# Optimization experiments

Hardware: AMD Instinct MI355X
Metric: run time of the kernel (lower is better)

Reference implementation:

```python
import jax, jax.numpy as jnp
import numpy as np

RATIOS = (0.5, 1.0, 2.0)
SCALES = (8.0, 16.0, 32.0)
FEAT_STRIDE = 16
BASE_SIZE = 16.0
NMS_THRESH = 0.7
N_PRE = 6000   # pre-NMS top-k (eval-mode ProposalCreator default)
N_POST = 300   # post-NMS proposals per image (eval-mode default)
MIN_SIZE = 16.0
SCALE = 1.0


def generate_anchor_base():
    ab = np.zeros((len(RATIOS) * len(SCALES), 4), np.float32)
    for i, r in enumerate(RATIOS):
        for j, s in enumerate(SCALES):
            h = BASE_SIZE * s * np.sqrt(r)
            w = BASE_SIZE * s * np.sqrt(1.0 / r)
            ab[i * len(SCALES) + j] = [-h / 2.0, -w / 2.0, h / 2.0, w / 2.0]
    return jnp.asarray(ab)


def enumerate_shifted_anchor(anchor_base, feat_stride, H, W):
    sy = jnp.arange(H, dtype=jnp.float32) * feat_stride
    sx = jnp.arange(W, dtype=jnp.float32) * feat_stride
    sx, sy = jnp.meshgrid(sx, sy)  # row-major over (y, x), matching torch permute order
    shift = jnp.stack([sy.ravel(), sx.ravel(), sy.ravel(), sx.ravel()], axis=1)  # [K,4]
    anchors = anchor_base[None, :, :] + shift[:, None, :]  # [K, A, 4]
    return anchors.reshape(-1, 4)


def loc2bbox(anchor, loc):
    # boxes in (y1, x1, y2, x2) format
    h = anchor[:, 2] - anchor[:, 0]
    w = anchor[:, 3] - anchor[:, 1]
    cy = anchor[:, 0] + 0.5 * h
    cx = anchor[:, 1] + 0.5 * w
    dy, dx, dh, dw = loc[:, 0], loc[:, 1], loc[:, 2], loc[:, 3]
    cy = cy + dy * h
    cx = cx + dx * w
    h = h * jnp.exp(dh)
    w = w * jnp.exp(dw)
    return jnp.stack([cy - 0.5 * h, cx - 0.5 * w, cy + 0.5 * h, cx + 0.5 * w], axis=1)


def nms_fixed(boxes, scores):
    # boxes [N_PRE,4] sorted desc by scores; greedy NMS emitting N_POST picks (padded)
    area = (boxes[:, 2] - boxes[:, 0]) * (boxes[:, 3] - boxes[:, 1])

    def step(sc, _):
        i = jnp.argmax(sc)
        v = sc[i] > -jnp.inf
        b = boxes[i]
        yy1 = jnp.maximum(boxes[:, 0], b[0])
        xx1 = jnp.maximum(boxes[:, 1], b[1])
        yy2 = jnp.minimum(boxes[:, 2], b[2])
        xx2 = jnp.minimum(boxes[:, 3], b[3])
        inter = jnp.maximum(yy2 - yy1, 0.0) * jnp.maximum(xx2 - xx1, 0.0)
        iou = inter / (area + area[i] - inter + 1e-9)
        sc = jnp.where((iou > NMS_THRESH) & v, -jnp.inf, sc)
        sc = sc.at[i].set(-jnp.inf)
        return sc, (i, v)

    _, (idx, valid) = jax.lax.scan(step, scores, None, length=N_POST)
    return jnp.where(valid[:, None], boxes[idx], 0.0)  # [N_POST, 4]


def proposal_one(loc, score, anchor, img_h, img_w):
    roi = loc2bbox(anchor, loc)
    roi = jnp.stack([
        jnp.clip(roi[:, 0], 0.0, img_h), jnp.clip(roi[:, 1], 0.0, img_w),
        jnp.clip(roi[:, 2], 0.0, img_h), jnp.clip(roi[:, 3], 0.0, img_w)], axis=1)
    hs = roi[:, 2] - roi[:, 0]
    ws = roi[:, 3] - roi[:, 1]
    min_size = MIN_SIZE * SCALE
    valid = (hs >= min_size) & (ws >= min_size)
    s = jnp.where(valid, score, -jnp.inf)
    top_s, top_i = jax.lax.top_k(s, N_PRE)
    return nms_fixed(roi[top_i], top_s)


def setup_inputs() -> dict:
    key = jax.random.key(0)
    ks = jax.random.split(key, 4)
    B, C, H, W = 8, 512, 64, 64
    A = 9
    return {
        "x": jax.random.normal(ks[0], (B, C, H, W), jnp.float32),
        "conv_w": jax.random.normal(ks[1], (C, C, 3, 3), jnp.float32) * 0.01,
        "conv_b": jnp.zeros((C,), jnp.float32),
        "loc_w": jax.random.normal(ks[2], (A * 4, C, 1, 1), jnp.float32) * 0.01,
        "loc_b": jnp.zeros((A * 4,), jnp.float32),
        "cls_w": jax.random.normal(ks[3], (A * 2, C, 1, 1), jnp.float32) * 0.01,
        "cls_b": jnp.zeros((A * 2,), jnp.float32),
        "img_h": 1024,
        "img_w": 1024,
    }


def reference(x, conv_w, conv_b, loc_w, loc_b, cls_w, cls_b, img_h, img_w):
    dn = ("NCHW", "OIHW", "NCHW")
    h = jax.lax.conv_general_dilated(x, conv_w, (1, 1), "SAME", dimension_numbers=dn)
    h = jax.nn.relu(h + conv_b[None, :, None, None])
    cls = jax.nn.sigmoid(
        jax.lax.conv_general_dilated(h, cls_w, (1, 1), "VALID", dimension_numbers=dn)
        + cls_b[None, :, None, None])
    loc = (jax.lax.conv_general_dilated(h, loc_w, (1, 1), "VALID", dimension_numbers=dn)
           + loc_b[None, :, None, None])
    B, _, H, W = h.shape
    anchor = enumerate_shifted_anchor(generate_anchor_base(), FEAT_STRIDE, H, W)
    pred_locations = loc.transpose(0, 2, 3, 1).reshape(B, -1, 4)          # [B, HWA, 4]
    cls_hw = cls.transpose(0, 2, 3, 1)                                     # [B, H, W, 2A]
    objectness = cls_hw.reshape(B, H, W, -1, 2)[..., 1].reshape(B, -1)     # [B, HWA]
    pred_cls_scores = cls_hw.reshape(B, -1, 2)                             # [B, HWA, 2]
    fh = jnp.float32(img_h)
    fw = jnp.float32(img_w)
    rois = jax.vmap(lambda l, s: proposal_one(l, s, anchor, fh, fw))(pred_locations, objectness)
    rois = rois.reshape(B * N_POST, 4)
    roi_indices = jnp.repeat(jnp.arange(B, dtype=jnp.int64 if jax.config.jax_enable_x64 else jnp.int32), N_POST)
    return pred_cls_scores, pred_locations, rois, roi_indices
```

## Files before the change

### kernel.cpp

```cpp
#include <hip/hip_runtime.h>
#include <cstdint>
#include <cmath>


#define AS1U(p) ((const __attribute__((address_space(1))) unsigned int*)(p))
#define AS3U(p) ((__attribute__((address_space(3))) unsigned int*)(p))

__global__ __launch_bounds__(256) void k_conv3x3(
        const float* __restrict__ x, const float* __restrict__ w,
        const float* __restrict__ bias, const float* __restrict__ zeropad,
        float* __restrict__ hout) {
    __shared__ __align__(16) float xs[8][6][68];
    __shared__ __align__(16) float wl[8][9][68];

    const int ytile = blockIdx.x;
    const int co0 = blockIdx.y * 64;
    const int b = blockIdx.z;
    const int t = threadIdx.x;
    const int xq = t & 7;
    const int coq = (t >> 3) & 7;
    const int yy = t >> 6;
    const int lane = t & 63;
    const int y0 = ytile * 4;

    if (t < 48) { int ci = t / 6, ry = t % 6; xs[ci][ry][0] = 0.f; xs[ci][ry][65] = 0.f; }

    float acc[8][8];
#pragma unroll
    for (int c = 0; c < 8; ++c)
#pragma unroll
        for (int i = 0; i < 8; ++i) acc[c][i] = 0.f;

    const int co_s = t >> 2, qs = t & 3;
    const float* wsrc = w + (size_t)(co0 + co_s) * 4608 + qs * 18;
    float* wrow = &wl[0][0][0] + (size_t)(2 * qs) * 9 * 68 + co_s;

    const int gy0 = y0 - 1;
    const float* xb = x + ((size_t)b * 512) * 4096;

    for (int ci0 = 0; ci0 < 512; ci0 += 8) {
        __syncthreads();
        {
#pragma unroll
            for (int j = 0; j < 12; ++j) {
                const int ci = 2 * yy + (j >= 6 ? 1 : 0);
                const int ry = (j >= 6) ? (j - 6) : j;
                const int gy = gy0 + ry;
                const float* src = (gy >= 0 && gy < 64)
                    ? xb + ((size_t)(ci0 + ci) * 64 + gy) * 64 + lane
                    : zeropad + lane;
                __builtin_amdgcn_global_load_lds(AS1U(src), AS3U(&xs[ci][ry][1]), 4, 0, 0);
            }
        }
        {
            const float2* wp2 = (const float2*)(wsrc + (size_t)ci0 * 9);
#pragma unroll
            for (int j2 = 0; j2 < 9; ++j2) {
                float2 f = wp2[j2];
                const int i0 = 2 * j2, i1 = 2 * j2 + 1;
                wrow[(i0 < 9 ? 0 : 9 * 68) + (i0 < 9 ? i0 : i0 - 9) * 68] = f.x;
                wrow[(i1 < 9 ? 0 : 9 * 68) + (i1 < 9 ? i1 : i1 - 9) * 68] = f.y;
            }
        }
        __syncthreads();
#pragma unroll
        for (int ci = 0; ci < 8; ++ci) {
#pragma unroll
            for (int ky = 0; ky < 3; ++ky) {
                const float* xr = &xs[ci][yy + ky][xq * 8];
                const float4 a0 = *(const float4*)(xr);
                const float4 a1 = *(const float4*)(xr + 4);
                const float2 a2 = *(const float2*)(xr + 8);
                float xw[10];
                xw[0] = a0.x; xw[1] = a0.y; xw[2] = a0.z; xw[3] = a0.w;
                xw[4] = a1.x; xw[5] = a1.y; xw[6] = a1.z; xw[7] = a1.w;
                xw[8] = a2.x; xw[9] = a2.y;
#pragma unroll
                for (int kx = 0; kx < 3; ++kx) {
                    const float4 w0 = *(const float4*)&wl[ci][ky * 3 + kx][coq * 8];
                    const float4 w1 = *(const float4*)&wl[ci][ky * 3 + kx][coq * 8 + 4];
#pragma unroll
                    for (int i = 0; i < 8; ++i) {
                        const float xv = xw[i + kx];
                        acc[0][i] += w0.x * xv; acc[1][i] += w0.y * xv;
                        acc[2][i] += w0.z * xv; acc[3][i] += w0.w * xv;
                        acc[4][i] += w1.x * xv; acc[5][i] += w1.y * xv;
                        acc[6][i] += w1.z * xv; acc[7][i] += w1.w * xv;
                    }
                }
            }
        }
    }
    const int y = y0 + yy;
#pragma unroll
    for (int c = 0; c < 8; ++c) {
        const int co = co0 + coq * 8 + c;
        const float bv = bias[co];
        float* op = hout + (((size_t)b * 512 + co) * 64 + y) * 64 + xq * 8;
        float4 o0, o1;
        o0.x = fmaxf(acc[c][0] + bv, 0.f); o0.y = fmaxf(acc[c][1] + bv, 0.f);
        o0.z = fmaxf(acc[c][2] + bv, 0.f); o0.w = fmaxf(acc[c][3] + bv, 0.f);
        o1.x = fmaxf(acc[c][4] + bv, 0.f); o1.y = fmaxf(acc[c][5] + bv, 0.f);
        o1.z = fmaxf(acc[c][6] + bv, 0.f); o1.w = fmaxf(acc[c][7] + bv, 0.f);
        *(float4*)(op) = o0;
        *(float4*)(op + 4) = o1;
    }
}

__global__ __launch_bounds__(128) void k_head(
        const float* __restrict__ h,
        const float* __restrict__ cls_w, const float* __restrict__ cls_b,
        const float* __restrict__ loc_w, const float* __restrict__ loc_b,
        const int* __restrict__ img_h_p, const int* __restrict__ img_w_p,
        float* __restrict__ out_cls, float* __restrict__ out_loc,
        float* __restrict__ boxes, float* __restrict__ scores) {
    const int tg = blockIdx.x * 128 + threadIdx.x;
    const int b = tg >> 12;
    const int pos = tg & 4095;
    const int y = pos >> 6, xc = pos & 63;
    float accC[18], accL[36];
#pragma unroll
    for (int o = 0; o < 18; ++o) accC[o] = 0.f;
#pragma unroll
    for (int o = 0; o < 36; ++o) accL[o] = 0.f;
    const float* hp = h + (size_t)b * 2097152 + pos;
#pragma unroll 4
    for (int ci = 0; ci < 512; ++ci) {
        const float hv = hp[(size_t)ci * 4096];
#pragma unroll
        for (int o = 0; o < 18; ++o) accC[o] += cls_w[o * 512 + ci] * hv;
#pragma unroll
        for (int o = 0; o < 36; ++o) accL[o] += loc_w[o * 512 + ci] * hv;
    }
    const float fh = (float)(*img_h_p);
    const float fw = (float)(*img_w_p);
    {
        const size_t obase = (size_t)b * 73728 + (size_t)pos * 18;
#pragma unroll
        for (int o = 0; o < 18; ++o) {
            accC[o] += cls_b[o];
            out_cls[obase + o] = 1.f / (1.f + expf(-accC[o]));
        }
    }
    {
        const size_t lbase = (size_t)b * 147456 + (size_t)pos * 36;
#pragma unroll
        for (int o = 0; o < 36; ++o) {
            accL[o] += loc_b[o];
            out_loc[lbase + o] = accL[o];
        }
    }
    const float sy = (float)(y * 16), sx = (float)(xc * 16);
    const double RR[3] = {0.5, 1.0, 2.0};
    const double SS[3] = {8.0, 16.0, 32.0};
#pragma unroll
    for (int a = 0; a < 9; ++a) {
        const double r = RR[a / 3], s = SS[a % 3];
        const double hd = 16.0 * s * sqrt(r);
        const double wd = 16.0 * s * sqrt(1.0 / r);
        const float ab0 = (float)(-hd / 2.0), ab1 = (float)(-wd / 2.0);
        const float ab2 = (float)(hd / 2.0), ab3 = (float)(wd / 2.0);
        const float a0 = ab0 + sy, a1 = ab1 + sx, a2 = ab2 + sy, a3 = ab3 + sx;
        float hh = a2 - a0, ww = a3 - a1;
        float cy = a0 + 0.5f * hh, cx = a1 + 0.5f * ww;
        const float dy = accL[a * 4 + 0], dx = accL[a * 4 + 1];
        const float dh = accL[a * 4 + 2], dw = accL[a * 4 + 3];
        cy = cy + dy * hh;
        cx = cx + dx * ww;
        hh = hh * expf(dh);
        ww = ww * expf(dw);
        float y1 = cy - 0.5f * hh, x1 = cx - 0.5f * ww;
        float y2 = cy + 0.5f * hh, x2 = cx + 0.5f * ww;
        y1 = fminf(fmaxf(y1, 0.f), fh); x1 = fminf(fmaxf(x1, 0.f), fw);
        y2 = fminf(fmaxf(y2, 0.f), fh); x2 = fminf(fmaxf(x2, 0.f), fw);
        const bool valid = ((y2 - y1) >= 16.f) && ((x2 - x1) >= 16.f);
        const float sc = 1.f / (1.f + expf(-accC[a * 2 + 1]));
        const int n = pos * 9 + a;
        float* bp = boxes + ((size_t)b * 36864 + n) * 4;
        bp[0] = y1; bp[1] = x1; bp[2] = y2; bp[3] = x2;
        scores[(size_t)b * 36864 + n] = valid ? sc : -INFINITY;
    }
}

__device__ __forceinline__ unsigned fmap(float f) {
    unsigned bits = __float_as_uint(f);
    return ((int)bits < 0) ? ~bits : (bits | 0x80000000u);
}

__global__ __launch_bounds__(1024) void k_select(
        const float* __restrict__ scores, unsigned* __restrict__ sel) {
    __shared__ unsigned hist[256];
    __shared__ unsigned tieL[1024];
    __shared__ unsigned sh_pref, sh_k, sh_cg, sh_ct;
    const int b = blockIdx.x;
    const int t = threadIdx.x;
    const int lane = t & 63;
    const unsigned long long lmlt = (1ull << lane) - 1ull;
    const float* sp = scores + (size_t)b * 36864;
    unsigned pref = 0;
    unsigned k = 6000;
    for (int p = 3; p >= 0; --p) {
        if (t < 256) hist[t] = 0;
        __syncthreads();
        const int sh = p * 8;
        for (int i = t; i < 36864; i += 1024) {
            unsigned u = fmap(sp[i]);
            bool match = (p == 3) || ((u >> (sh + 8)) == (pref >> (sh + 8)));
            unsigned bin = (u >> sh) & 255u;
            unsigned long long act = __ballot(match);
            while (act) {
                int lead = __ffsll((unsigned long long)act) - 1;
                unsigned lbin = __shfl(bin, lead, 64);
                unsigned long long same = __ballot(match && (bin == lbin));
                if (lane == lead) atomicAdd(&hist[lbin], (unsigned)__popcll(same));
                act &= ~same;
            }
        }
        __syncthreads();
        if (t == 0) {
            unsigned c = 0;
            int bsel = 0;
            for (int bin = 255; bin >= 0; --bin) {
                unsigned c2 = c + hist[bin];
                if (c2 >= k) { bsel = bin; k = k - c; break; }
                c = c2;
            }
            pref |= ((unsigned)bsel) << sh;
            sh_pref = pref; sh_k = k;
        }
        __syncthreads();
        pref = sh_pref; k = sh_k;
        __syncthreads();
    }
    if (t == 0) { sh_cg = 0; sh_ct = 0; }
    __syncthreads();
    const unsigned uthr = pref;
    for (int i = t; i < 36864; i += 1024) {
        unsigned u = fmap(sp[i]);
        const bool g = (u > uthr);
        const bool e = (u == uthr);
        unsigned long long bg = __ballot(g);
        if (bg) {
            int lead = __ffsll((unsigned long long)bg) - 1;
            unsigned basev = 0;
            if (lane == lead) basev = atomicAdd(&sh_cg, (unsigned)__popcll(bg));
            basev = __shfl(basev, lead, 64);
            if (g) sel[(size_t)b * 6000 + basev + (unsigned)__popcll(bg & lmlt)] = (unsigned)i;
        }
        unsigned long long be = __ballot(e);
        if (be) {
            int lead = __ffsll((unsigned long long)be) - 1;
            unsigned baset = 0;
            if (lane == lead) baset = atomicAdd(&sh_ct, (unsigned)__popcll(be));
            baset = __shfl(baset, lead, 64);
            if (e) {
                unsigned tp = baset + (unsigned)__popcll(be & lmlt);
                if (tp < 1024) tieL[tp] = (unsigned)i;
            }
        }
    }
    __syncthreads();
    const unsigned G = sh_cg;
    const unsigned T = sh_ct;
    const unsigned need = k;
    const unsigned Tc = T < 1024u ? T : 1024u;
    if ((unsigned)t >= Tc) tieL[t] = 0xFFFFFFFFu;
    __syncthreads();
    if (need > 0) {
        if (T > 1) {
            for (int kk = 2; kk <= 1024; kk <<= 1) {
                for (int j = kk >> 1; j > 0; j >>= 1) {
                    int ixj = t ^ j;
                    if (ixj > t) {
                        unsigned va = tieL[t], vb = tieL[ixj];
                        bool up = ((t & kk) == 0);
                        if (up ? (va > vb) : (va < vb)) { tieL[t] = vb; tieL[ixj] = va; }
                    }
                    __syncthreads();
                }
            }
        }
        if ((unsigned)t < need) sel[(size_t)b * 6000 + G + t] = tieL[t];
    }
}

__global__ __launch_bounds__(1024) void k_nms(
        const float* __restrict__ boxes, const float* __restrict__ scores,
        const unsigned* __restrict__ sel,
        float* __restrict__ rois, float* __restrict__ roi_idx) {
    __shared__ unsigned long long warr[16];
    __shared__ unsigned long long winK;
    const int b = blockIdx.x;
    const int t = threadIdx.x;
    const unsigned UNEG = 0x007FFFFFu;
    float bx[6][4];
    unsigned long long key[6];
#pragma unroll
    for (int j = 0; j < 6; ++j) {
        int s = t + j * 1024;
        if (s < 6000) {
            unsigned idx = sel[(size_t)b * 6000 + s];
            const float* bp = boxes + ((size_t)b * 36864 + idx) * 4;
            bx[j][0] = bp[0]; bx[j][1] = bp[1]; bx[j][2] = bp[2]; bx[j][3] = bp[3];
            unsigned u = fmap(scores[(size_t)b * 36864 + idx]);
            key[j] = ((unsigned long long)u << 32) | (unsigned)(~idx);
        } else {
            key[j] = 0ull;
            bx[j][0] = bx[j][1] = bx[j][2] = bx[j][3] = 0.f;
        }
    }
    const int lane = t & 63;
    const int wid = t >> 6;
    float* orow = rois + (size_t)b * 300 * 4;
    for (int k = 0; k < 300; ++k) {
        unsigned long long m = key[0];
#pragma unroll
        for (int j = 1; j < 6; ++j) m = key[j] > m ? key[j] : m;
#pragma unroll
        for (int d = 32; d > 0; d >>= 1) {
            unsigned long long o = __shfl_xor(m, d, 64);
            if (o > m) m = o;
        }
        if (lane == 0) warr[wid] = m;
        __syncthreads();
        if (t == 0) {
            unsigned long long wv = warr[0];
#pragma unroll
            for (int i = 1; i < 16; ++i) if (warr[i] > wv) wv = warr[i];
            winK = wv;
        }
        __syncthreads();
        const unsigned long long wk = winK;
        const unsigned uhi = (unsigned)(wk >> 32);
        if (uhi > UNEG) {
            const unsigned widx = ~(unsigned)wk;
            const float* bp = boxes + ((size_t)b * 36864 + widx) * 4;
            const float py1 = bp[0], px1 = bp[1], py2 = bp[2], px2 = bp[3];
            const float parea = (py2 - py1) * (px2 - px1);
            if (t == 0) {
                orow[k * 4 + 0] = py1; orow[k * 4 + 1] = px1;
                orow[k * 4 + 2] = py2; orow[k * 4 + 3] = px2;
                roi_idx[b * 300 + k] = (float)b;
            }
#pragma unroll
            for (int j = 0; j < 6; ++j) {
                if ((unsigned)(key[j] >> 32) > UNEG) {
                    float yy1 = fmaxf(bx[j][0], py1);
                    float xx1 = fmaxf(bx[j][1], px1);
                    float yy2 = fminf(bx[j][2], py2);
                    float xx2 = fminf(bx[j][3], px2);
                    float inter = fmaxf(yy2 - yy1, 0.f) * fmaxf(xx2 - xx1, 0.f);
                    float area = (bx[j][2] - bx[j][0]) * (bx[j][3] - bx[j][1]);
                    float iou = inter / (area + parea - inter + 1e-9f);
                    if (iou > 0.7f)
                        key[j] = ((unsigned long long)UNEG << 32) | (key[j] & 0xFFFFFFFFull);
                }
            }
        } else {
            if (t == 0) {
                orow[k * 4 + 0] = 0.f; orow[k * 4 + 1] = 0.f;
                orow[k * 4 + 2] = 0.f; orow[k * 4 + 3] = 0.f;
                roi_idx[b * 300 + k] = (float)b;
            }
        }
        __syncthreads();
    }
}

extern "C" void kernel_launch(void* const* d_in, const int* in_sizes, int n_in,
                              void* d_out, int out_size, void* d_ws, size_t ws_size,
                              hipStream_t stream) {
    (void)in_sizes; (void)n_in; (void)out_size; (void)ws_size;
    const float* x      = (const float*)d_in[0];
    const float* conv_w = (const float*)d_in[1];
    const float* conv_b = (const float*)d_in[2];
    const float* loc_w  = (const float*)d_in[3];
    const float* loc_b  = (const float*)d_in[4];
    const float* cls_w  = (const float*)d_in[5];
    const float* cls_b  = (const float*)d_in[6];
    const int* img_h    = (const int*)d_in[7];
    const int* img_w    = (const int*)d_in[8];

    char* ws = (char*)d_ws;
    float*    h      = (float*)(ws + 0);
    float*    boxes  = (float*)(ws + 67108864);
    float*    scores = (float*)(ws + 71827456);
    unsigned* sel    = (unsigned*)(ws + 73007104);
    float*    zp     = (float*)(ws + 73199104);

    float* out      = (float*)d_out;
    float* out_cls  = out;
    float* out_loc  = out + 589824;
    float* rois     = out + 1769472;
    float* ridx     = out + 1779072;

    hipMemsetAsync(zp, 0, 256, stream);
    k_conv3x3<<<dim3(16, 8, 8), 256, 0, stream>>>(x, conv_w, conv_b, zp, h);
    k_head<<<dim3(256), 128, 0, stream>>>(h, cls_w, cls_b, loc_w, loc_b,
                                          img_h, img_w, out_cls, out_loc, boxes, scores);
    k_select<<<dim3(8), 1024, 0, stream>>>(scores, sel);
    k_nms<<<dim3(8), 1024, 0, stream>>>(boxes, scores, sel, rois, ridx);
}
```

Measured before the change: 3.248 ms.

## Pre-transpose conv weights for async LDS loads; trim select and NMS syncs

Adds a kernel that transposes the 3x3 conv weights to a [ci*9][co] layout, so the conv kernel can stream weights straight into LDS with global_load_lds instead of staging them through registers with strided stores. The old conv path is kept as a fallback when the workspace is too small. It also raises the unroll factor in the head's channel loop, and switches the top-k histogram to per-wave LDS histograms with plain atomics in place of the ballot/shuffle loop. NMS double-buffers its per-wave max array so every thread does the final reduction, which removes one barrier and the single-thread reduction each iteration. The transpose adds an extra launch and weight traffic on every call.

```diff
diff --git a/kernel.cpp b/kernel.cpp
--- a/kernel.cpp
+++ b/kernel.cpp
@@ -6,8 +6,15 @@
 #define AS1U(p) ((const __attribute__((address_space(1))) unsigned int*)(p))
 #define AS3U(p) ((__attribute__((address_space(3))) unsigned int*)(p))
 
-__global__ __launch_bounds__(256) void k_conv3x3(
-        const float* __restrict__ x, const float* __restrict__ w,
+__global__ __launch_bounds__(512) void k_wtrans(
+        const float* __restrict__ w, float* __restrict__ wT) {
+    const int cik = blockIdx.x;
+    const int co = threadIdx.x;
+    wT[(size_t)cik * 512 + co] = w[(size_t)co * 4608 + cik];
+}
+
+__global__ __launch_bounds__(256) void k_conv3x3_wt(
+        const float* __restrict__ x, const float* __restrict__ wT,
         const float* __restrict__ bias, const float* __restrict__ zeropad,
         float* __restrict__ hout) {
     __shared__ __align__(16) float xs[8][6][68];
@@ -31,26 +38,112 @@
 #pragma unroll
         for (int i = 0; i < 8; ++i) acc[c][i] = 0.f;
 
+    const int gy0 = y0 - 1;
+    const float* xb = x + ((size_t)b * 512) * 4096;
+
+    for (int ci0 = 0; ci0 < 512; ci0 += 8) {
+        __syncthreads();
+#pragma unroll
+        for (int j = 0; j < 12; ++j) {
+            const int ci = 2 * yy + (j >= 6 ? 1 : 0);
+            const int ry = (j >= 6) ? (j - 6) : j;
+            const int gy = gy0 + ry;
+            const float* src = (gy >= 0 && gy < 64)
+                ? xb + ((size_t)(ci0 + ci) * 64 + gy) * 64 + lane
+                : zeropad + lane;
+            __builtin_amdgcn_global_load_lds(AS1U(src), AS3U(&xs[ci][ry][1]), 4, 0, 0);
+        }
+#pragma unroll
+        for (int c2 = 0; c2 < 2; ++c2) {
+            const int cil = 2 * yy + c2;
+#pragma unroll
+            for (int k = 0; k < 9; ++k) {
+                const float* src = wT + ((size_t)(ci0 + cil) * 9 + k) * 512 + co0 + lane;
+                __builtin_amdgcn_global_load_lds(AS1U(src), AS3U(&wl[cil][k][0]), 4, 0, 0);
+            }
+        }
+        __syncthreads();
+#pragma unroll
+        for (int ci = 0; ci < 8; ++ci) {
+#pragma unroll
+            for (int ky = 0; ky < 3; ++ky) {
+                const float* xr = &xs[ci][yy + ky][xq * 8];
+                const float4 a0 = *(const float4*)(xr);
+                const float4 a1 = *(const float4*)(xr + 4);
+                const float2 a2 = *(const float2*)(xr + 8);
+                float xw[10];
+                xw[0] = a0.x; xw[1] = a0.y; xw[2] = a0.z; xw[3] = a0.w;
+                xw[4] = a1.x; xw[5] = a1.y; xw[6] = a1.z; xw[7] = a1.w;
+                xw[8] = a2.x; xw[9] = a2.y;
+#pragma unroll
+                for (int kx = 0; kx < 3; ++kx) {
+                    const float4 w0 = *(const float4*)&wl[ci][ky * 3 + kx][coq * 8];
+                    const float4 w1 = *(const float4*)&wl[ci][ky * 3 + kx][coq * 8 + 4];
+#pragma unroll
+                    for (int i = 0; i < 8; ++i) {
+                        const float xv = xw[i + kx];
+                        acc[0][i] += w0.x * xv; acc[1][i] += w0.y * xv;
+                        acc[2][i] += w0.z * xv; acc[3][i] += w0.w * xv;
+                        acc[4][i] += w1.x * xv; acc[5][i] += w1.y * xv;
+                        acc[6][i] += w1.z * xv; acc[7][i] += w1.w * xv;
+                    }
+                }
+            }
+        }
+    }
+    const int y = y0 + yy;
+#pragma unroll
+    for (int c = 0; c < 8; ++c) {
+        const int co = co0 + coq * 8 + c;
+        const float bv = bias[co];
+        float* op = hout + (((size_t)b * 512 + co) * 64 + y) * 64 + xq * 8;
+        float4 o0, o1;
+        o0.x = fmaxf(acc[c][0] + bv, 0.f); o0.y = fmaxf(acc[c][1] + bv, 0.f);
+        o0.z = fmaxf(acc[c][2] + bv, 0.f); o0.w = fmaxf(acc[c][3] + bv, 0.f);
+        o1.x = fmaxf(acc[c][4] + bv, 0.f); o1.y = fmaxf(acc[c][5] + bv, 0.f);
+        o1.z = fmaxf(acc[c][6] + bv, 0.f); o1.w = fmaxf(acc[c][7] + bv, 0.f);
+        *(float4*)(op) = o0;
+        *(float4*)(op + 4) = o1;
+    }
+}
+
+__global__ __launch_bounds__(256) void k_conv3x3(
+        const float* __restrict__ x, const float* __restrict__ w,
+        const float* __restrict__ bias, const float* __restrict__ zeropad,
+        float* __restrict__ hout) {
+    __shared__ __align__(16) float xs[8][6][68];
+    __shared__ __align__(16) float wl[8][9][68];
+    const int ytile = blockIdx.x;
+    const int co0 = blockIdx.y * 64;
+    const int b = blockIdx.z;
+    const int t = threadIdx.x;
+    const int xq = t & 7;
+    const int coq = (t >> 3) & 7;
+    const int yy = t >> 6;
+    const int lane = t & 63;
+    const int y0 = ytile * 4;
+    if (t < 48) { int ci = t / 6, ry = t % 6; xs[ci][ry][0] = 0.f; xs[ci][ry][65] = 0.f; }
+    float acc[8][8];
+#pragma unroll
+    for (int c = 0; c < 8; ++c)
+#pragma unroll
+        for (int i = 0; i < 8; ++i) acc[c][i] = 0.f;
     const int co_s = t >> 2, qs = t & 3;
     const float* wsrc = w + (size_t)(co0 + co_s) * 4608 + qs * 18;
     float* wrow = &wl[0][0][0] + (size_t)(2 * qs) * 9 * 68 + co_s;
-
     const int gy0 = y0 - 1;
     const float* xb = x + ((size_t)b * 512) * 4096;
-
     for (int ci0 = 0; ci0 < 512; ci0 += 8) {
         __syncthreads();
-        {
-#pragma unroll
-            for (int j = 0; j < 12; ++j) {
-                const int ci = 2 * yy + (j >= 6 ? 1 : 0);
-                const int ry = (j >= 6) ? (j - 6) : j;
-                const int gy = gy0 + ry;
-                const float* src = (gy >= 0 && gy < 64)
-                    ? xb + ((size_t)(ci0 + ci) * 64 + gy) * 64 + lane
-                    : zeropad + lane;
-                __builtin_amdgcn_global_load_lds(AS1U(src), AS3U(&xs[ci][ry][1]), 4, 0, 0);
-            }
+#pragma unroll
+        for (int j = 0; j < 12; ++j) {
+            const int ci = 2 * yy + (j >= 6 ? 1 : 0);
+            const int ry = (j >= 6) ? (j - 6) : j;
+            const int gy = gy0 + ry;
+            const float* src = (gy >= 0 && gy < 64)
+                ? xb + ((size_t)(ci0 + ci) * 64 + gy) * 64 + lane
+                : zeropad + lane;
+            __builtin_amdgcn_global_load_lds(AS1U(src), AS3U(&xs[ci][ry][1]), 4, 0, 0);
         }
         {
             const float2* wp2 = (const float2*)(wsrc + (size_t)ci0 * 9);
@@ -124,7 +217,7 @@
 #pragma unroll
     for (int o = 0; o < 36; ++o) accL[o] = 0.f;
     const float* hp = h + (size_t)b * 2097152 + pos;
-#pragma unroll 4
+#pragma unroll 8
     for (int ci = 0; ci < 512; ++ci) {
         const float hv = hp[(size_t)ci * 4096];
 #pragma unroll
@@ -189,32 +282,33 @@
 
 __global__ __launch_bounds__(1024) void k_select(
         const float* __restrict__ scores, unsigned* __restrict__ sel) {
+    __shared__ unsigned h2[16][256];
     __shared__ unsigned hist[256];
     __shared__ unsigned tieL[1024];
     __shared__ unsigned sh_pref, sh_k, sh_cg, sh_ct;
     const int b = blockIdx.x;
     const int t = threadIdx.x;
     const int lane = t & 63;
+    const int wid = t >> 6;
     const unsigned long long lmlt = (1ull << lane) - 1ull;
     const float* sp = scores + (size_t)b * 36864;
     unsigned pref = 0;
     unsigned k = 6000;
     for (int p = 3; p >= 0; --p) {
-        if (t < 256) hist[t] = 0;
+        for (int z = t; z < 4096; z += 1024) ((unsigned*)h2)[z] = 0;
         __syncthreads();
         const int sh = p * 8;
         for (int i = t; i < 36864; i += 1024) {
             unsigned u = fmap(sp[i]);
             bool match = (p == 3) || ((u >> (sh + 8)) == (pref >> (sh + 8)));
-            unsigned bin = (u >> sh) & 255u;
-            unsigned long long act = __ballot(match);
-            while (act) {
-                int lead = __ffsll((unsigned long long)act) - 1;
-                unsigned lbin = __shfl(bin, lead, 64);
-                unsigned long long same = __ballot(match && (bin == lbin));
-                if (lane == lead) atomicAdd(&hist[lbin], (unsigned)__popcll(same));
-                act &= ~same;
-            }
+            if (match) atomicAdd(&h2[wid][(u >> sh) & 255u], 1u);
+        }
+        __syncthreads();
+        if (t < 256) {
+            unsigned s = 0;
+#pragma unroll
+            for (int j = 0; j < 16; ++j) s += h2[j][t];
+            hist[t] = s;
         }
         __syncthreads();
         if (t == 0) {
@@ -288,8 +382,7 @@
         const float* __restrict__ boxes, const float* __restrict__ scores,
         const unsigned* __restrict__ sel,
         float* __restrict__ rois, float* __restrict__ roi_idx) {
-    __shared__ unsigned long long warr[16];
-    __shared__ unsigned long long winK;
+    __shared__ unsigned long long warr[2][16];
     const int b = blockIdx.x;
     const int t = threadIdx.x;
     const unsigned UNEG = 0x007FFFFFu;
@@ -313,6 +406,7 @@
     const int wid = t >> 6;
     float* orow = rois + (size_t)b * 300 * 4;
     for (int k = 0; k < 300; ++k) {
+        const int pb = k & 1;
         unsigned long long m = key[0];
 #pragma unroll
         for (int j = 1; j < 6; ++j) m = key[j] > m ? key[j] : m;
@@ -321,16 +415,11 @@
             unsigned long long o = __shfl_xor(m, d, 64);
             if (o > m) m = o;
         }
-        if (lane == 0) warr[wid] = m;
-        __syncthreads();
-        if (t == 0) {
-            unsigned long long wv = warr[0];
-#pragma unroll
-            for (int i = 1; i < 16; ++i) if (warr[i] > wv) wv = warr[i];
-            winK = wv;
-        }
-        __syncthreads();
-        const unsigned long long wk = winK;
+        if (lane == 0) warr[pb][wid] = m;
+        __syncthreads();
+        unsigned long long wk = warr[pb][0];
+#pragma unroll
+        for (int i = 1; i < 16; ++i) { unsigned long long v = warr[pb][i]; if (v > wk) wk = v; }
         const unsigned uhi = (unsigned)(wk >> 32);
         if (uhi > UNEG) {
             const unsigned widx = ~(unsigned)wk;
@@ -363,14 +452,13 @@
                 roi_idx[b * 300 + k] = (float)b;
             }
         }
-        __syncthreads();
     }
 }
 
 extern "C" void kernel_launch(void* const* d_in, const int* in_sizes, int n_in,
                               void* d_out, int out_size, void* d_ws, size_t ws_size,
                               hipStream_t stream) {
-    (void)in_sizes; (void)n_in; (void)out_size; (void)ws_size;
+    (void)in_sizes; (void)n_in; (void)out_size;
     const float* x      = (const float*)d_in[0];
     const float* conv_w = (const float*)d_in[1];
     const float* conv_b = (const float*)d_in[2];
@@ -387,6 +475,7 @@
     float*    scores = (float*)(ws + 71827456);
     unsigned* sel    = (unsigned*)(ws + 73007104);
     float*    zp     = (float*)(ws + 73199104);
+    float*    wT     = (float*)(ws + 73199360);
 
     float* out      = (float*)d_out;
     float* out_cls  = out;
@@ -394,8 +483,15 @@
     float* rois     = out + 1769472;
     float* ridx     = out + 1779072;
 
+    const bool big_ws = (ws_size >= 82636544ull);
+
     hipMemsetAsync(zp, 0, 256, stream);
-    k_conv3x3<<<dim3(16, 8, 8), 256, 0, stream>>>(x, conv_w, conv_b, zp, h);
+    if (big_ws) {
+        k_wtrans<<<dim3(4608), 512, 0, stream>>>(conv_w, wT);
+        k_conv3x3_wt<<<dim3(16, 8, 8), 256, 0, stream>>>(x, wT, conv_b, zp, h);
+    } else {
+        k_conv3x3<<<dim3(16, 8, 8), 256, 0, stream>>>(x, conv_w, conv_b, zp, h);
+    }
     k_head<<<dim3(256), 128, 0, stream>>>(h, cls_w, cls_b, loc_w, loc_b,
                                           img_h, img_w, out_cls, out_loc, boxes, scores);
     k_select<<<dim3(8), 1024, 0, stream>>>(scores, sel);
```

New measurement: 3.357 ms. 3.4% more time.
